# Optimization experiments

Measured on AMD Instinct MI355X. Metric: run time of the kernel, lower is better.

## Reference

```python
import jax, jax.numpy as jnp
import numpy as np

B, S, D, H = 2, 2048, 2048, 16
DPH = D // H  # 128


def setup_inputs() -> dict:
    key = jax.random.key(0)
    k1, _ = jax.random.split(key)
    query = jax.random.normal(k1, (B, S, D), dtype=jnp.float32)
    mask = jnp.ones((B, S), dtype=jnp.int32)  # True = allow attention
    return {"query": query, "mask": mask}


def reference(query, mask):
    # Faithful to the given snippet: q_lin/k_lin/v_lin/out_lin are defined in
    # __init__ but never invoked in forward, and attn_mask is constructed but
    # never applied to dot_prod. Self-attention path: key = value = query.
    b, q_len, dim = query.shape
    scale = np.sqrt(DPH).astype(np.float32)

    # prepare_head: [B, S, D] -> [B, H, S, dph]
    q = query.reshape(b, q_len, H, DPH).transpose(0, 2, 1, 3) / scale
    k = query.reshape(b, q_len, H, DPH).transpose(0, 2, 1, 3)
    v = k

    # dot_prod = (q/scale) @ k^T : [B, H, Sq, Sk]
    dot_prod = jnp.einsum('bhqd,bhkd->bhqk', q, k)

    # fp32 softmax, cast back to query dtype (mask is NOT applied in source)
    attn_weights = jax.nn.softmax(dot_prod.astype(jnp.float32), axis=-1).astype(query.dtype)

    attentioned = jnp.einsum('bhqk,bhkd->bhqd', attn_weights, v)
    out = attentioned.transpose(0, 2, 1, 3).reshape(b, q_len, dim)

    # new_incr_state tensors (prev_key/prev_value in [B, H, S, dph], prev_mask)
    prev_key = k.reshape(b, H, q_len, DPH)
    prev_value = v.reshape(b, H, q_len, DPH)
    # dot_prod returned as [B*H, Sq, Sk] to match source shape
    return out, prev_key, prev_value, mask, dot_prod.reshape(b * H, q_len, q_len)
```

## Files before the change

### kernel.cpp

```cpp
#include <hip/hip_runtime.h>
#include <hip/hip_bf16.h>

#define BB 2
#define HH 16
#define SS 2048
#define DD 2048
#define DPH_ 128
#define QBLK 128
#define KBLK 64
#define NT (SS / KBLK)

#define KSTR 136
#define VSTR 72
#define PSTR 72

typedef __bf16 bf16x8 __attribute__((ext_vector_type(8)));
typedef unsigned short u16x8 __attribute__((ext_vector_type(8)));
typedef float f32x4 __attribute__((ext_vector_type(4)));

__device__ __forceinline__ unsigned short f2bfbits(float f) {
  unsigned u = __builtin_bit_cast(unsigned, f);
  u += 0x7FFFu + ((u >> 16) & 1u);
  return (unsigned short)(u >> 16);
}
__device__ __forceinline__ __bf16 f2bf(float f) {
  unsigned short s = f2bfbits(f);
  return __builtin_bit_cast(__bf16, s);
}
__device__ __forceinline__ void nt_store4(const float4& v, float* p) {
  f32x4 t = {v.x, v.y, v.z, v.w};
  __builtin_nontemporal_store(t, (f32x4*)p);
}

template <bool PRE>
__global__ __launch_bounds__(256)
void preproc(const float* __restrict__ q, const int* __restrict__ mask,
             __bf16* __restrict__ qb, float* __restrict__ omask) {
  const size_t i = (size_t)blockIdx.x * 256 + threadIdx.x;
  const size_t e = i * 8;
  if constexpr (PRE) {
    const float4 v0 = *(const float4*)(q + e);
    const float4 v1 = *(const float4*)(q + e + 4);
    u16x8 t;
    t[0] = f2bfbits(v0.x); t[1] = f2bfbits(v0.y);
    t[2] = f2bfbits(v0.z); t[3] = f2bfbits(v0.w);
    t[4] = f2bfbits(v1.x); t[5] = f2bfbits(v1.y);
    t[6] = f2bfbits(v1.z); t[7] = f2bfbits(v1.w);
    *(u16x8*)(qb + e) = t;
  }
  if (i < (size_t)BB * SS) omask[i] = (float)mask[i];
}

template <bool PRE>
__global__ __launch_bounds__(512, 4)
void attn_fused(const __bf16* __restrict__ qb, const float* __restrict__ qf,
                float* __restrict__ out, float* __restrict__ dot,
                float* __restrict__ pk, float* __restrict__ pv) {
  __shared__ __bf16 kls[KBLK * KSTR];
  __shared__ __bf16 vls[DPH_ * VSTR];
  __shared__ __bf16 pls[8 * 16 * PSTR];

  const int bid = blockIdx.x;
  const int xcd = bid & 7;
  const int t_  = bid >> 3;
  const int qt  = t_ & 15;
  const int G   = (t_ >> 4) * 8 + xcd;
  const int h   = G & 15;
  const int b   = G >> 4;

  const int tid  = threadIdx.x;
  const int wid  = tid >> 6;
  const int lane = tid & 63;
  const int g    = lane >> 4;
  const int c    = lane & 15;
  const int skv  = lane;

  const int qbase = qt * QBLK;
  const float scale = 0.08838834764831845f;

  const size_t headoff = (size_t)b * SS * DD + (size_t)h * DPH_;
  const __bf16* qbh = PRE ? qb + headoff : nullptr;
  const float*  qfh = qf + headoff;

  bf16x8 aq[4];
  {
    const int row = qbase + wid * 16 + c;
    if constexpr (PRE) {
      const __bf16* p = qbh + (size_t)row * DD + 8 * g;
      #pragma unroll
      for (int st = 0; st < 4; ++st) aq[st] = *(const bf16x8*)(p + st * 32);
    } else {
      const float* p = qfh + (size_t)row * DD + 8 * g;
      #pragma unroll
      for (int st = 0; st < 4; ++st) {
        u16x8 t;
        #pragma unroll
        for (int i2 = 0; i2 < 8; ++i2) t[i2] = f2bfbits(p[st * 32 + i2]);
        aq[st] = __builtin_bit_cast(bf16x8, t);
      }
    }
  }

  auto load_tile = [&](int kvb, bf16x8& a0, bf16x8& a1) {
    if constexpr (PRE) {
      const __bf16* p = qbh + (size_t)(kvb + skv) * DD + wid * 8;
      a0 = *(const bf16x8*)p;
      a1 = *(const bf16x8*)(p + 64);
    } else {
      const float* p = qfh + (size_t)(kvb + skv) * DD + wid * 8;
      const float4 f0 = *(const float4*)p;
      const float4 f1 = *(const float4*)(p + 4);
      const float4 f2 = *(const float4*)(p + 64);
      const float4 f3 = *(const float4*)(p + 68);
      u16x8 t0, t1;
      t0[0] = f2bfbits(f0.x); t0[1] = f2bfbits(f0.y);
      t0[2] = f2bfbits(f0.z); t0[3] = f2bfbits(f0.w);
      t0[4] = f2bfbits(f1.x); t0[5] = f2bfbits(f1.y);
      t0[6] = f2bfbits(f1.z); t0[7] = f2bfbits(f1.w);
      t1[0] = f2bfbits(f2.x); t1[1] = f2bfbits(f2.y);
      t1[2] = f2bfbits(f2.z); t1[3] = f2bfbits(f2.w);
      t1[4] = f2bfbits(f3.x); t1[5] = f2bfbits(f3.y);
      t1[6] = f2bfbits(f3.z); t1[7] = f2bfbits(f3.w);
      a0 = __builtin_bit_cast(bf16x8, t0);
      a1 = __builtin_bit_cast(bf16x8, t1);
    }
  };
  auto write_tile = [&](bf16x8 a0, bf16x8 a1) {
    *(bf16x8*)(&kls[skv * KSTR + wid * 8]) = a0;
    *(bf16x8*)(&kls[skv * KSTR + (wid + 8) * 8]) = a1;
    #pragma unroll
    for (int j = 0; j < 8; ++j) {
      vls[(wid * 8 + j) * VSTR + skv] = a0[j];
      vls[((wid + 8) * 8 + j) * VSTR + skv] = a1[j];
    }
  };

  const f32x4 zero4 = {0.f, 0.f, 0.f, 0.f};
  f32x4 o[8];
  #pragma unroll
  for (int t = 0; t < 8; ++t) o[t] = zero4;
  float m[4], l[4];
  #pragma unroll
  for (int r = 0; r < 4; ++r) { m[r] = -1e30f; l[r] = 0.0f; }

  float* __restrict__ dotb = dot + ((size_t)(b * HH + h) << 22);

  bf16x8 p0, p1;
  load_tile(0, p0, p1);
  write_tile(p0, p1);
  __syncthreads();

  for (int kt = 0; kt < NT; ++kt) {
    const int kvbase = kt * KBLK;

    f32x4 s[4];
    #pragma unroll
    for (int ct = 0; ct < 4; ++ct) s[ct] = zero4;
    __builtin_amdgcn_s_setprio(1);
    #pragma unroll
    for (int st = 0; st < 4; ++st) {
      #pragma unroll
      for (int ct = 0; ct < 4; ++ct) {
        bf16x8 bk = *(const bf16x8*)(&kls[(ct * 16 + c) * KSTR + st * 32 + 8 * g]);
        s[ct] = __builtin_amdgcn_mfma_f32_16x16x32_bf16(aq[st], bk, s[ct], 0, 0, 0);
      }
    }
    __builtin_amdgcn_s_setprio(0);

    if (kt + 1 < NT) load_tile(kvbase + KBLK, p0, p1);

    #pragma unroll
    for (int ct = 0; ct < 4; ++ct) s[ct] *= scale;
    #pragma unroll
    for (int r = 0; r < 4; ++r) {
      float* dp = dotb + (size_t)(qbase + wid * 16 + 4 * g + r) * SS + kvbase + c;
      #pragma unroll
      for (int ct = 0; ct < 4; ++ct)
        __builtin_nontemporal_store(s[ct][r], dp + ct * 16);
    }

    float alpha[4];
    #pragma unroll
    for (int r = 0; r < 4; ++r) {
      float tm = fmaxf(fmaxf(s[0][r], s[1][r]), fmaxf(s[2][r], s[3][r]));
      #pragma unroll
      for (int off = 1; off < 16; off <<= 1) tm = fmaxf(tm, __shfl_xor(tm, off));
      float mn = fmaxf(m[r], tm);
      alpha[r] = __expf(m[r] - mn);
      m[r] = mn;
    }
    float rs[4] = {0.f, 0.f, 0.f, 0.f};
    #pragma unroll
    for (int ct = 0; ct < 4; ++ct) {
      #pragma unroll
      for (int r = 0; r < 4; ++r) {
        float p = __expf(s[ct][r] - m[r]);
        s[ct][r] = p;
        rs[r] += p;
      }
    }
    #pragma unroll
    for (int r = 0; r < 4; ++r) {
      #pragma unroll
      for (int off = 1; off < 16; off <<= 1) rs[r] += __shfl_xor(rs[r], off);
      l[r] = l[r] * alpha[r] + rs[r];
      #pragma unroll
      for (int t = 0; t < 8; ++t) o[t][r] *= alpha[r];
    }

    {
      __bf16* pw = &pls[wid * 16 * PSTR];
      #pragma unroll
      for (int ct = 0; ct < 4; ++ct)
        #pragma unroll
        for (int r = 0; r < 4; ++r)
          pw[(4 * g + r) * PSTR + ct * 16 + c] = f2bf(s[ct][r]);
    }

    __builtin_amdgcn_s_setprio(1);
    #pragma unroll
    for (int kk = 0; kk < 2; ++kk) {
      bf16x8 ap = *(const bf16x8*)(&pls[(wid * 16 + c) * PSTR + kk * 32 + 8 * g]);
      #pragma unroll
      for (int t = 0; t < 8; ++t) {
        bf16x8 bv = *(const bf16x8*)(&vls[(t * 16 + c) * VSTR + kk * 32 + 8 * g]);
        o[t] = __builtin_amdgcn_mfma_f32_16x16x32_bf16(ap, bv, o[t], 0, 0, 0);
      }
    }
    __builtin_amdgcn_s_setprio(0);

    __syncthreads();
    if (kt + 1 < NT) write_tile(p0, p1);
    __syncthreads();
  }

  #pragma unroll
  for (int r = 0; r < 4; ++r) {
    float inv = 1.0f / l[r];
    float* op = out + (size_t)(b * SS + qbase + wid * 16 + 4 * g + r) * DD + h * DPH_ + c;
    #pragma unroll
    for (int t = 0; t < 8; ++t)
      __builtin_nontemporal_store(o[t][r] * inv, op + t * 16);
  }

  {
    const size_t bh = (size_t)b * HH + h;
    const int col = (tid & 31) * 4;
    #pragma unroll
    for (int rr = 0; rr < QBLK; rr += 16) {
      const int row = qbase + rr + (tid >> 5);
      const float4 v = *(const float4*)(qfh + (size_t)row * DD + col);
      nt_store4(v, pk + (bh * SS + row) * DPH_ + col);
      nt_store4(v, pv + (bh * SS + row) * DPH_ + col);
    }
  }
}

extern "C" void kernel_launch(void* const* d_in, const int* in_sizes, int n_in,
                              void* d_out, int out_size, void* d_ws, size_t ws_size,
                              hipStream_t stream) {
  const float* q    = (const float*)d_in[0];
  const int*   mask = (const int*)d_in[1];
  float* out = (float*)d_out;

  float* o_out  = out;
  float* o_pk   = out + 8388608;
  float* o_pv   = out + 16777216;
  float* o_mask = out + 25165824;
  float* o_dot  = out + 25169920;

  const size_t need = (size_t)BB * SS * DD * sizeof(__bf16);
  const dim3 agrid(512);

  if (ws_size >= need) {
    __bf16* qbf = (__bf16*)d_ws;
    preproc<true><<<4096, 256, 0, stream>>>(q, mask, qbf, o_mask);
    attn_fused<true><<<agrid, 512, 0, stream>>>(qbf, q, o_out, o_dot, o_pk, o_pv);
  } else {
    preproc<false><<<4096, 256, 0, stream>>>(q, mask, nullptr, o_mask);
    attn_fused<false><<<agrid, 512, 0, stream>>>(nullptr, q, o_out, o_dot, o_pk, o_pv);
  }
}
```

Measured before the change: 195.1 us.

## Use 4 waves with 32 query rows each to reuse K/V fragments

```diff
diff --git a/kernel.cpp b/kernel.cpp
--- a/kernel.cpp
+++ b/kernel.cpp
@@ -17,11 +17,15 @@
 typedef __bf16 bf16x8 __attribute__((ext_vector_type(8)));
 typedef unsigned short u16x8 __attribute__((ext_vector_type(8)));
 typedef float f32x4 __attribute__((ext_vector_type(4)));
-
-__device__ __forceinline__ unsigned short f2bfbits(float f) {
+typedef unsigned int u32x4 __attribute__((ext_vector_type(4)));
+
+__device__ __forceinline__ unsigned f2bfbits32(float f) {
   unsigned u = __builtin_bit_cast(unsigned, f);
   u += 0x7FFFu + ((u >> 16) & 1u);
-  return (unsigned short)(u >> 16);
+  return u >> 16;
+}
+__device__ __forceinline__ unsigned short f2bfbits(float f) {
+  return (unsigned short)f2bfbits32(f);
 }
 __device__ __forceinline__ __bf16 f2bf(float f) {
   unsigned short s = f2bfbits(f);
@@ -52,13 +56,13 @@
 }
 
 template <bool PRE>
-__global__ __launch_bounds__(512, 4)
+__global__ __launch_bounds__(256, 2)
 void attn_fused(const __bf16* __restrict__ qb, const float* __restrict__ qf,
                 float* __restrict__ out, float* __restrict__ dot,
                 float* __restrict__ pk, float* __restrict__ pv) {
   __shared__ __bf16 kls[KBLK * KSTR];
   __shared__ __bf16 vls[DPH_ * VSTR];
-  __shared__ __bf16 pls[8 * 16 * PSTR];
+  __shared__ __bf16 pls[4 * 32 * PSTR];
 
   const int bid = blockIdx.x;
   const int xcd = bid & 7;
@@ -73,7 +77,6 @@
   const int lane = tid & 63;
   const int g    = lane >> 4;
   const int c    = lane & 15;
-  const int skv  = lane;
 
   const int qbase = qt * QBLK;
   const float scale = 0.08838834764831845f;
@@ -82,13 +85,14 @@
   const __bf16* qbh = PRE ? qb + headoff : nullptr;
   const float*  qfh = qf + headoff;
 
-  bf16x8 aq[4];
-  {
-    const int row = qbase + wid * 16 + c;
+  bf16x8 aq[2][4];
+  #pragma unroll
+  for (int u = 0; u < 2; ++u) {
+    const int row = qbase + wid * 32 + u * 16 + c;
     if constexpr (PRE) {
       const __bf16* p = qbh + (size_t)row * DD + 8 * g;
       #pragma unroll
-      for (int st = 0; st < 4; ++st) aq[st] = *(const bf16x8*)(p + st * 32);
+      for (int st = 0; st < 4; ++st) aq[u][st] = *(const bf16x8*)(p + st * 32);
     } else {
       const float* p = qfh + (size_t)row * DD + 8 * g;
       #pragma unroll
@@ -96,159 +100,190 @@
         u16x8 t;
         #pragma unroll
         for (int i2 = 0; i2 < 8; ++i2) t[i2] = f2bfbits(p[st * 32 + i2]);
-        aq[st] = __builtin_bit_cast(bf16x8, t);
-      }
-    }
-  }
-
-  auto load_tile = [&](int kvb, bf16x8& a0, bf16x8& a1) {
+        aq[u][st] = __builtin_bit_cast(bf16x8, t);
+      }
+    }
+  }
+
+  const int p2 = tid & 31;
+  const int oo = tid >> 5;
+  const int r0 = 2 * p2;
+
+  bf16x8 st0, st1, st2, st3;
+  auto load_tile = [&](int kvb) {
     if constexpr (PRE) {
-      const __bf16* p = qbh + (size_t)(kvb + skv) * DD + wid * 8;
-      a0 = *(const bf16x8*)p;
-      a1 = *(const bf16x8*)(p + 64);
+      const __bf16* pA = qbh + (size_t)(kvb + r0) * DD + 16 * oo;
+      st0 = *(const bf16x8*)pA;
+      st1 = *(const bf16x8*)(pA + 8);
+      st2 = *(const bf16x8*)(pA + DD);
+      st3 = *(const bf16x8*)(pA + DD + 8);
     } else {
-      const float* p = qfh + (size_t)(kvb + skv) * DD + wid * 8;
-      const float4 f0 = *(const float4*)p;
-      const float4 f1 = *(const float4*)(p + 4);
-      const float4 f2 = *(const float4*)(p + 64);
-      const float4 f3 = *(const float4*)(p + 68);
-      u16x8 t0, t1;
-      t0[0] = f2bfbits(f0.x); t0[1] = f2bfbits(f0.y);
-      t0[2] = f2bfbits(f0.z); t0[3] = f2bfbits(f0.w);
-      t0[4] = f2bfbits(f1.x); t0[5] = f2bfbits(f1.y);
-      t0[6] = f2bfbits(f1.z); t0[7] = f2bfbits(f1.w);
-      t1[0] = f2bfbits(f2.x); t1[1] = f2bfbits(f2.y);
-      t1[2] = f2bfbits(f2.z); t1[3] = f2bfbits(f2.w);
-      t1[4] = f2bfbits(f3.x); t1[5] = f2bfbits(f3.y);
-      t1[6] = f2bfbits(f3.z); t1[7] = f2bfbits(f3.w);
-      a0 = __builtin_bit_cast(bf16x8, t0);
-      a1 = __builtin_bit_cast(bf16x8, t1);
+      const float* pA = qfh + (size_t)(kvb + r0) * DD + 16 * oo;
+      u16x8 t0, t1, t2, t3;
+      #pragma unroll
+      for (int i2 = 0; i2 < 8; ++i2) {
+        t0[i2] = f2bfbits(pA[i2]);
+        t1[i2] = f2bfbits(pA[8 + i2]);
+        t2[i2] = f2bfbits(pA[DD + i2]);
+        t3[i2] = f2bfbits(pA[DD + 8 + i2]);
+      }
+      st0 = __builtin_bit_cast(bf16x8, t0);
+      st1 = __builtin_bit_cast(bf16x8, t1);
+      st2 = __builtin_bit_cast(bf16x8, t2);
+      st3 = __builtin_bit_cast(bf16x8, t3);
     }
   };
-  auto write_tile = [&](bf16x8 a0, bf16x8 a1) {
-    *(bf16x8*)(&kls[skv * KSTR + wid * 8]) = a0;
-    *(bf16x8*)(&kls[skv * KSTR + (wid + 8) * 8]) = a1;
+  auto write_tile = [&]() {
+    *(bf16x8*)(&kls[r0 * KSTR + 16 * oo])       = st0;
+    *(bf16x8*)(&kls[r0 * KSTR + 16 * oo + 8])   = st1;
+    *(bf16x8*)(&kls[(r0+1) * KSTR + 16 * oo])     = st2;
+    *(bf16x8*)(&kls[(r0+1) * KSTR + 16 * oo + 8]) = st3;
+    const unsigned* a0 = (const unsigned*)&st0;
+    const unsigned* a1 = (const unsigned*)&st1;
+    const unsigned* b0 = (const unsigned*)&st2;
+    const unsigned* b1 = (const unsigned*)&st3;
     #pragma unroll
     for (int j = 0; j < 8; ++j) {
-      vls[(wid * 8 + j) * VSTR + skv] = a0[j];
-      vls[((wid + 8) * 8 + j) * VSTR + skv] = a1[j];
+      unsigned loA = (j < 4 ? a0[j] : a1[j - 4]);
+      unsigned loB = (j < 4 ? b0[j] : b1[j - 4]);
+      unsigned w0 = (loA & 0xFFFFu) | (loB << 16);
+      unsigned w1 = (loA >> 16) | (loB & 0xFFFF0000u);
+      *(unsigned*)(&vls[(16 * oo + 2 * j) * VSTR + r0]) = w0;
+      *(unsigned*)(&vls[(16 * oo + 2 * j + 1) * VSTR + r0]) = w1;
     }
   };
 
   const f32x4 zero4 = {0.f, 0.f, 0.f, 0.f};
-  f32x4 o[8];
+  f32x4 o[2][8];
   #pragma unroll
-  for (int t = 0; t < 8; ++t) o[t] = zero4;
-  float m[4], l[4];
+  for (int u = 0; u < 2; ++u)
+    #pragma unroll
+    for (int t = 0; t < 8; ++t) o[u][t] = zero4;
+  float m[2][4], l[2][4];
   #pragma unroll
-  for (int r = 0; r < 4; ++r) { m[r] = -1e30f; l[r] = 0.0f; }
+  for (int u = 0; u < 2; ++u)
+    #pragma unroll
+    for (int r = 0; r < 4; ++r) { m[u][r] = -1e30f; l[u][r] = 0.0f; }
 
   float* __restrict__ dotb = dot + ((size_t)(b * HH + h) << 22);
 
-  bf16x8 p0, p1;
-  load_tile(0, p0, p1);
-  write_tile(p0, p1);
+  load_tile(0);
+  write_tile();
   __syncthreads();
 
   for (int kt = 0; kt < NT; ++kt) {
     const int kvbase = kt * KBLK;
 
-    f32x4 s[4];
-    #pragma unroll
-    for (int ct = 0; ct < 4; ++ct) s[ct] = zero4;
+    f32x4 s[2][4];
+    #pragma unroll
+    for (int u = 0; u < 2; ++u)
+      #pragma unroll
+      for (int ct = 0; ct < 4; ++ct) s[u][ct] = zero4;
     __builtin_amdgcn_s_setprio(1);
     #pragma unroll
     for (int st = 0; st < 4; ++st) {
       #pragma unroll
       for (int ct = 0; ct < 4; ++ct) {
         bf16x8 bk = *(const bf16x8*)(&kls[(ct * 16 + c) * KSTR + st * 32 + 8 * g]);
-        s[ct] = __builtin_amdgcn_mfma_f32_16x16x32_bf16(aq[st], bk, s[ct], 0, 0, 0);
+        #pragma unroll
+        for (int u = 0; u < 2; ++u)
+          s[u][ct] = __builtin_amdgcn_mfma_f32_16x16x32_bf16(aq[u][st], bk, s[u][ct], 0, 0, 0);
       }
     }
     __builtin_amdgcn_s_setprio(0);
 
-    if (kt + 1 < NT) load_tile(kvbase + KBLK, p0, p1);
-
-    #pragma unroll
-    for (int ct = 0; ct < 4; ++ct) s[ct] *= scale;
-    #pragma unroll
-    for (int r = 0; r < 4; ++r) {
-      float* dp = dotb + (size_t)(qbase + wid * 16 + 4 * g + r) * SS + kvbase + c;
+    if (kt + 1 < NT) load_tile(kvbase + KBLK);
+
+    #pragma unroll
+    for (int u = 0; u < 2; ++u) {
+      #pragma unroll
+      for (int ct = 0; ct < 4; ++ct) s[u][ct] *= scale;
+      #pragma unroll
+      for (int r = 0; r < 4; ++r) {
+        float* dp = dotb + (size_t)(qbase + wid * 32 + u * 16 + 4 * g + r) * SS + kvbase + c;
+        #pragma unroll
+        for (int ct = 0; ct < 4; ++ct)
+          __builtin_nontemporal_store(s[u][ct][r], dp + ct * 16);
+      }
+    }
+
+    #pragma unroll
+    for (int u = 0; u < 2; ++u) {
+      float alpha[4];
+      #pragma unroll
+      for (int r = 0; r < 4; ++r) {
+        float tm = fmaxf(fmaxf(s[u][0][r], s[u][1][r]), fmaxf(s[u][2][r], s[u][3][r]));
+        #pragma unroll
+        for (int off = 1; off < 16; off <<= 1) tm = fmaxf(tm, __shfl_xor(tm, off));
+        float mn = fmaxf(m[u][r], tm);
+        alpha[r] = __expf(m[u][r] - mn);
+        m[u][r] = mn;
+      }
+      float rs[4] = {0.f, 0.f, 0.f, 0.f};
+      #pragma unroll
+      for (int ct = 0; ct < 4; ++ct) {
+        #pragma unroll
+        for (int r = 0; r < 4; ++r) {
+          float p = __expf(s[u][ct][r] - m[u][r]);
+          s[u][ct][r] = p;
+          rs[r] += p;
+        }
+      }
+      #pragma unroll
+      for (int r = 0; r < 4; ++r) {
+        #pragma unroll
+        for (int off = 1; off < 16; off <<= 1) rs[r] += __shfl_xor(rs[r], off);
+        l[u][r] = l[u][r] * alpha[r] + rs[r];
+        #pragma unroll
+        for (int t = 0; t < 8; ++t) o[u][t][r] *= alpha[r];
+      }
+      __bf16* pw = &pls[wid * 32 * PSTR];
       #pragma unroll
       for (int ct = 0; ct < 4; ++ct)
-        __builtin_nontemporal_store(s[ct][r], dp + ct * 16);
-    }
-
-    float alpha[4];
-    #pragma unroll
-    for (int r = 0; r < 4; ++r) {
-      float tm = fmaxf(fmaxf(s[0][r], s[1][r]), fmaxf(s[2][r], s[3][r]));
-      #pragma unroll
-      for (int off = 1; off < 16; off <<= 1) tm = fmaxf(tm, __shfl_xor(tm, off));
-      float mn = fmaxf(m[r], tm);
-      alpha[r] = __expf(m[r] - mn);
-      m[r] = mn;
-    }
-    float rs[4] = {0.f, 0.f, 0.f, 0.f};
-    #pragma unroll
-    for (int ct = 0; ct < 4; ++ct) {
-      #pragma unroll
-      for (int r = 0; r < 4; ++r) {
-        float p = __expf(s[ct][r] - m[r]);
-        s[ct][r] = p;
-        rs[r] += p;
-      }
-    }
-    #pragma unroll
-    for (int r = 0; r < 4; ++r) {
-      #pragma unroll
-      for (int off = 1; off < 16; off <<= 1) rs[r] += __shfl_xor(rs[r], off);
-      l[r] = l[r] * alpha[r] + rs[r];
-      #pragma unroll
-      for (int t = 0; t < 8; ++t) o[t][r] *= alpha[r];
-    }
-
-    {
-      __bf16* pw = &pls[wid * 16 * PSTR];
-      #pragma unroll
-      for (int ct = 0; ct < 4; ++ct)
         #pragma unroll
         for (int r = 0; r < 4; ++r)
-          pw[(4 * g + r) * PSTR + ct * 16 + c] = f2bf(s[ct][r]);
+          pw[(u * 16 + 4 * g + r) * PSTR + ct * 16 + c] = f2bf(s[u][ct][r]);
     }
 
     __builtin_amdgcn_s_setprio(1);
     #pragma unroll
     for (int kk = 0; kk < 2; ++kk) {
-      bf16x8 ap = *(const bf16x8*)(&pls[(wid * 16 + c) * PSTR + kk * 32 + 8 * g]);
+      bf16x8 ap[2];
+      #pragma unroll
+      for (int u = 0; u < 2; ++u)
+        ap[u] = *(const bf16x8*)(&pls[wid * 32 * PSTR + (u * 16 + c) * PSTR + kk * 32 + 8 * g]);
       #pragma unroll
       for (int t = 0; t < 8; ++t) {
         bf16x8 bv = *(const bf16x8*)(&vls[(t * 16 + c) * VSTR + kk * 32 + 8 * g]);
-        o[t] = __builtin_amdgcn_mfma_f32_16x16x32_bf16(ap, bv, o[t], 0, 0, 0);
+        #pragma unroll
+        for (int u = 0; u < 2; ++u)
+          o[u][t] = __builtin_amdgcn_mfma_f32_16x16x32_bf16(ap[u], bv, o[u][t], 0, 0, 0);
       }
     }
     __builtin_amdgcn_s_setprio(0);
 
     __syncthreads();
-    if (kt + 1 < NT) write_tile(p0, p1);
+    if (kt + 1 < NT) write_tile();
     __syncthreads();
   }
 
   #pragma unroll
-  for (int r = 0; r < 4; ++r) {
-    float inv = 1.0f / l[r];
-    float* op = out + (size_t)(b * SS + qbase + wid * 16 + 4 * g + r) * DD + h * DPH_ + c;
-    #pragma unroll
-    for (int t = 0; t < 8; ++t)
-      __builtin_nontemporal_store(o[t][r] * inv, op + t * 16);
-  }
+  for (int u = 0; u < 2; ++u)
+    #pragma unroll
+    for (int r = 0; r < 4; ++r) {
+      float inv = 1.0f / l[u][r];
+      float* op = out + (size_t)(b * SS + qbase + wid * 32 + u * 16 + 4 * g + r) * DD + h * DPH_ + c;
+      #pragma unroll
+      for (int t = 0; t < 8; ++t)
+        __builtin_nontemporal_store(o[u][t][r] * inv, op + t * 16);
+    }
 
   {
     const size_t bh = (size_t)b * HH + h;
     const int col = (tid & 31) * 4;
     #pragma unroll
-    for (int rr = 0; rr < QBLK; rr += 16) {
-      const int row = qbase + rr + (tid >> 5);
+    for (int rr = 0; rr < 16; ++rr) {
+      const int row = qbase + rr * 8 + (tid >> 5);
       const float4 v = *(const float4*)(qfh + (size_t)row * DD + col);
       nt_store4(v, pk + (bh * SS + row) * DPH_ + col);
       nt_store4(v, pv + (bh * SS + row) * DPH_ + col);
@@ -275,9 +310,9 @@
   if (ws_size >= need) {
     __bf16* qbf = (__bf16*)d_ws;
     preproc<true><<<4096, 256, 0, stream>>>(q, mask, qbf, o_mask);
-    attn_fused<true><<<agrid, 512, 0, stream>>>(qbf, q, o_out, o_dot, o_pk, o_pv);
+    attn_fused<true><<<agrid, 256, 0, stream>>>(qbf, q, o_out, o_dot, o_pk, o_pv);
   } else {
     preproc<false><<<4096, 256, 0, stream>>>(q, mask, nullptr, o_mask);
-    attn_fused<false><<<agrid, 512, 0, stream>>>(nullptr, q, o_out, o_dot, o_pk, o_pv);
-  }
-}
+    attn_fused<false><<<agrid, 256, 0, stream>>>(nullptr, q, o_out, o_dot, o_pk, o_pv);
+  }
+}
```

Result: faster. 185.8 us (-4.8%).
